# Kernel tuning notes

Hardware: AMD Instinct MI355X
Metric: run time of the kernel (lower is better)

The kernel has to match this reference:

```python
import jax, jax.numpy as jnp
import numpy as np

D_MODEL = 1024
NUM_HEADS = 4
KEY_DIM = 1024      # dim * expand_k
VALUE_DIM = 2048    # dim * expand_v
HEAD_QK = KEY_DIM // NUM_HEADS   # 256
HEAD_V = VALUE_DIM // NUM_HEADS  # 512
EPS = 1e-5
ROPE_BASE = 10000.0
XAVIER_GAIN = 2.0 ** (-2.5)


def _xavier_uniform(key, shape, gain=XAVIER_GAIN):
    fan_in, fan_out = shape
    a = gain * np.sqrt(6.0 / (fan_in + fan_out))
    return jax.random.uniform(key, shape, jnp.float32, -a, a)


def setup_inputs() -> dict:
    key = jax.random.key(0)
    ks = jax.random.split(key, 5)
    x = jax.random.normal(ks[0], (2, 2048, D_MODEL), jnp.float32)
    # stored as (in, out); y = x @ W matches torch Linear(no bias) with W^T
    Wq = _xavier_uniform(ks[1], (D_MODEL, KEY_DIM))
    Wk = _xavier_uniform(ks[2], (D_MODEL, KEY_DIM))
    Wv = _xavier_uniform(ks[3], (D_MODEL, VALUE_DIM))
    Wo = _xavier_uniform(ks[4], (VALUE_DIM, D_MODEL))
    return {"x": x, "Wq": Wq, "Wk": Wk, "Wv": Wv, "Wo": Wo}


def _rope(t, base=ROPE_BASE):
    # t: [b, n, h, d]; standard half-split rotary embedding
    n, d = t.shape[1], t.shape[-1]
    half = d // 2
    inv_freq = 1.0 / (base ** (jnp.arange(0, half, dtype=jnp.float32) * 2.0 / d))
    ang = jnp.arange(n, dtype=jnp.float32)[:, None] * inv_freq  # [n, d/2]
    cos = jnp.cos(ang)[None, :, None, :]
    sin = jnp.sin(ang)[None, :, None, :]
    t1, t2 = t[..., :half], t[..., half:]
    return jnp.concatenate([t1 * cos - t2 * sin, t2 * cos + t1 * sin], axis=-1)


def reference(x, Wq, Wk, Wv, Wo):
    b, n, _ = x.shape
    # projections: b n (h d) -> b (n) h d
    q = (x @ Wq).reshape(b, n, NUM_HEADS, HEAD_QK)
    k = (x @ Wk).reshape(b, n, NUM_HEADS, HEAD_QK)
    v = (x @ Wv).reshape(b, n, NUM_HEADS, HEAD_V).transpose(0, 2, 1, 3)  # b h n dv
    q = _rope(q).transpose(0, 2, 1, 3)  # b h n dk
    k = _rope(k).transpose(0, 2, 1, 3)
    scale = HEAD_QK ** (-0.5)
    exp_qk = jnp.tril(jnp.exp(jnp.einsum('bhid,bhjd->bhij', q, k) * scale))
    exp_kk = jnp.tril(jnp.exp(jnp.einsum('bhid,bhjd->bhij', k, k) * scale))
    A = exp_kk.astype(jnp.float32) + EPS * jnp.eye(n, dtype=jnp.float32)
    sol = jax.lax.linalg.triangular_solve(A, v.astype(jnp.float32),
                                          left_side=True, lower=True)
    o = exp_qk.astype(jnp.float32) @ sol                # b h n dv
    o = o.transpose(0, 2, 1, 3).reshape(b, n, VALUE_DIM)  # b n (h dv)
    return o.astype(x.dtype) @ Wo
```

## Files before the change

### kernel.cpp

```cpp
#include <hip/hip_runtime.h>
#include <hip/hip_bf16.h>
#include <math.h>

#define SEQ   2048
#define NROW  4096
#define DM    1024
#define LDQ   1024
#define LDV   2048
#define NBLK  16

typedef float  f32x4  __attribute__((ext_vector_type(4)));
typedef int    i32x4  __attribute__((ext_vector_type(4)));
typedef __bf16 bf16x8 __attribute__((ext_vector_type(8)));

#define MFMA(d, a, b) (d) = __builtin_amdgcn_mfma_f32_16x16x32_bf16((a), (b), (d), 0, 0, 0)

__device__ inline ushort f2bf(float f) {
  __hip_bfloat16 h = __float2bfloat16(f);
  return *(ushort*)&h;
}
__device__ inline float bf2f(ushort u) {
  return __uint_as_float((unsigned)u << 16);
}
__device__ inline void split2(float v, ushort& hi, ushort& lo) {
  hi = f2bf(v);
  lo = f2bf(v - bf2f(hi));
}
__device__ inline bf16x8 ldfrag(const ushort* p) { return *(const bf16x8*)p; }

__device__ inline void gload_lds16(const ushort* g, ushort* l) {
  __builtin_amdgcn_global_load_lds(
      (const __attribute__((address_space(1))) void*)g,
      (__attribute__((address_space(3))) void*)l, 16, 0, 0);
}

__global__ void pack_x_kernel(const float* __restrict__ X, ushort* __restrict__ P)
{
  const int t = blockIdx.x * 256 + threadIdx.x;
  const int kc = t & 127;
  const int m  = t >> 7;
  const float* src = X + (size_t)m * DM + kc * 8;
  f32x4 v0 = *(const f32x4*)src;
  f32x4 v1 = *(const f32x4*)(src + 4);
  ushort o[8];
  #pragma unroll
  for (int j = 0; j < 4; ++j) { o[j] = f2bf(v0[j]); o[4 + j] = f2bf(v1[j]); }
  ushort* dst = P + ((size_t)((m >> 7) * 128 + kc) * 128 + (m & 127)) * 8;
  *(i32x4*)dst = *(i32x4*)o;
}

__global__ void pack_w_kernel(const float* __restrict__ W, ushort* __restrict__ P,
                              int K, int N)
{
  const int K8 = K >> 3;
  const int t = blockIdx.x * 256 + threadIdx.x;
  const int c  = t & 127;
  const int kc = (t >> 7) % K8;
  const int nb = t / (128 * K8);
  ushort o[8];
  #pragma unroll
  for (int j = 0; j < 8; ++j)
    o[j] = f2bf(W[(size_t)(kc * 8 + j) * N + nb * 128 + c]);
  ushort* dst = P + ((size_t)(nb * K8 + kc) * 128 + c) * 8;
  *(i32x4*)dst = *(i32x4*)o;
}

__global__ void pack_w2_kernel(const float* __restrict__ Wq, const float* __restrict__ Wk,
                               ushort* __restrict__ Pq, ushort* __restrict__ Pk)
{
  const float* W = blockIdx.y ? Wk : Wq;
  ushort* P      = blockIdx.y ? Pk : Pq;
  const int K8 = 128;
  const int t = blockIdx.x * 256 + threadIdx.x;
  const int c  = t & 127;
  const int kc = (t >> 7) % K8;
  const int nb = t / (128 * K8);
  ushort o[8];
  #pragma unroll
  for (int j = 0; j < 8; ++j)
    o[j] = f2bf(W[(size_t)(kc * 8 + j) * 1024 + nb * 128 + c]);
  ushort* dst = P + ((size_t)(nb * K8 + kc) * 128 + c) * 8;
  *(i32x4*)dst = *(i32x4*)o;
}

__global__ void rope_pack1_kernel(const float* __restrict__ M,
                                  ushort* __restrict__ Phi, ushort* __restrict__ Plo)
{
  const int idx = blockIdx.x * 256 + threadIdx.x;
  const int g   = idx & 31;
  const int h   = (idx >> 5) & 3;
  const int row = idx >> 7;
  const int pos = row & (SEQ - 1);
  const int d0  = g * 8;
  const bool hihalf = d0 >= 128;
  const int f0 = d0 & 127;
  const float* mp = M + (size_t)row * LDQ + h * 256;
  ushort oh[8], ol[8];
  #pragma unroll
  for (int j = 0; j < 8; ++j) {
    const int f = f0 + j;
    const float inv = expf(-(float)f * (9.210340371976184f / 128.f));
    float s, c;
    sincosf((float)pos * inv, &s, &c);
    const float m1 = mp[f], m2 = mp[f + 128];
    const float mv = hihalf ? (m2 * c + m1 * s) : (m1 * c - m2 * s);
    split2(mv, oh[j], ol[j]);
  }
  const int b = row >> 11, r = row & 127, tb = (row & 2047) >> 7;
  const int bh = b * 4 + h;
  const size_t doff = (((size_t)(bh * 16 + tb) * 32 + g) * 128 + r) * 8;
  *(i32x4*)(Phi + doff) = *(i32x4*)oh;
  *(i32x4*)(Plo + doff) = *(i32x4*)ol;
}

__global__ void pack_sol_kernel(const float* __restrict__ Vb, ushort* __restrict__ Sp)
{
  const int hj = blockIdx.x;
  const int h  = hj >> 4, jb = hj & 15;
  const int c  = blockIdx.y * 256 + threadIdx.x;
  const float* src = Vb + (size_t)(jb * 128) * LDV + h * 512 + c;
  ushort* dhi = Sp + ((size_t)hj * 2    ) * 65536;
  ushort* dlo = Sp + ((size_t)hj * 2 + 1) * 65536;
  for (int kc = 0; kc < 16; ++kc) {
    ushort oh[8], ol[8];
    #pragma unroll
    for (int j = 0; j < 8; ++j)
      split2(src[(size_t)(kc * 8 + j) * LDV], oh[j], ol[j]);
    *(i32x4*)(dhi + ((size_t)kc * 512 + c) * 8) = *(i32x4*)oh;
    *(i32x4*)(dlo + ((size_t)kc * 512 + c) * 8) = *(i32x4*)ol;
  }
}

__global__ __launch_bounds__(256) void gemm_bf16(
    const ushort* __restrict__ Ap, const ushort* __restrict__ Bp,
    float* __restrict__ C, int M, int N, int K)
{
  __shared__ __align__(16) ushort a_lds[8][128][8];
  __shared__ __align__(16) ushort b_lds[8][128][8];
  const int tid  = threadIdx.x;
  const int lane = tid & 63;
  const int w    = tid >> 6;
  const int wr   = w >> 1, wc = w & 1;
  const int mb = blockIdx.y, nb = blockIdx.x;
  const int K8 = K >> 3;
  const ushort* aT = Ap + (size_t)mb * K8 * 1024;
  const ushort* bT = Bp + (size_t)nb * K8 * 1024;
  const int lr = lane & 15;
  const int lk = lane >> 4;

  f32x4 acc[4][4];
  #pragma unroll
  for (int i = 0; i < 4; ++i)
    #pragma unroll
    for (int j = 0; j < 4; ++j) acc[i][j] = (f32x4)(0.f);

  for (int kc0 = 0; kc0 < K8; kc0 += 8) {
    const ushort* asrc = aT + (size_t)kc0 * 1024;
    const ushort* bsrc = bT + (size_t)kc0 * 1024;
    __syncthreads();
    #pragma unroll
    for (int it = 0; it < 4; ++it) {
      gload_lds16(asrc + it * 2048 + tid * 8, ((ushort*)a_lds) + it * 2048 + tid * 8);
      gload_lds16(bsrc + it * 2048 + tid * 8, ((ushort*)b_lds) + it * 2048 + tid * 8);
    }
    __syncthreads();
    #pragma unroll
    for (int kk = 0; kk < 2; ++kk) {
      bf16x8 af[4], bf[4];
      #pragma unroll
      for (int m = 0; m < 4; ++m)
        af[m] = ldfrag(&a_lds[kk * 4 + lk][wr * 64 + m * 16 + lr][0]);
      #pragma unroll
      for (int n = 0; n < 4; ++n)
        bf[n] = ldfrag(&b_lds[kk * 4 + lk][wc * 64 + n * 16 + lr][0]);
      #pragma unroll
      for (int m = 0; m < 4; ++m)
        #pragma unroll
        for (int n = 0; n < 4; ++n)
          MFMA(acc[m][n], af[m], bf[n]);
    }
  }
  const int r0 = (lane >> 4) * 4;
  #pragma unroll
  for (int m = 0; m < 4; ++m)
    #pragma unroll
    for (int n = 0; n < 4; ++n) {
      const int row = mb * 128 + wr * 64 + m * 16 + r0;
      const int col = nb * 128 + wc * 64 + n * 16 + lr;
      float* cp = C + (size_t)row * N + col;
      #pragma unroll
      for (int q = 0; q < 4; ++q) cp[(size_t)q * N] = acc[m][n][q];
    }
}

__global__ __launch_bounds__(256) void winv_kernel(
    const ushort* __restrict__ Khi, const ushort* __restrict__ Klo,
    ushort* __restrict__ Whi, ushort* __restrict__ Wlo)
{
  __shared__ float L[128][129];
  __shared__ float W[128][129];
  const int t = blockIdx.x, bh = blockIdx.y;
  const int tid = threadIdx.x;
  const int lane = tid & 63, w = tid >> 6;
  const int wr = w >> 1, wc = w & 1;
  const int lr = lane & 15, lk = lane >> 4;
  const size_t kb = (size_t)(bh * 16 + t) * 32768;

  f32x4 acc[4][4];
  #pragma unroll
  for (int i = 0; i < 4; ++i)
    #pragma unroll
    for (int j = 0; j < 4; ++j) acc[i][j] = (f32x4)(0.f);
  #pragma unroll
  for (int ks = 0; ks < 8; ++ks) {
    bf16x8 ah[4], al[4];
    #pragma unroll
    for (int m = 0; m < 4; ++m) {
      const size_t off = kb + ((size_t)(ks * 4 + lk) * 128 + wr * 64 + m * 16 + lr) * 8;
      ah[m] = ldfrag(Khi + off);
      al[m] = ldfrag(Klo + off);
    }
    #pragma unroll
    for (int n = 0; n < 4; ++n) {
      const size_t off = kb + ((size_t)(ks * 4 + lk) * 128 + wc * 64 + n * 16 + lr) * 8;
      bf16x8 bh_ = ldfrag(Khi + off);
      bf16x8 bl_ = ldfrag(Klo + off);
      #pragma unroll
      for (int m = 0; m < 4; ++m) {
        MFMA(acc[m][n], ah[m], bh_);
        MFMA(acc[m][n], ah[m], bl_);
        MFMA(acc[m][n], al[m], bh_);
      }
    }
  }
  for (int i = tid; i < 128 * 129; i += 256) ((float*)W)[i] = 0.f;
  #pragma unroll
  for (int m = 0; m < 4; ++m)
    #pragma unroll
    for (int n = 0; n < 4; ++n)
      #pragma unroll
      for (int q = 0; q < 4; ++q) {
        const int row = wr * 64 + m * 16 + lk * 4 + q;
        const int col = wc * 64 + n * 16 + lr;
        float v = __expf(acc[m][n][q] * 0.0625f);
        if (row == col) v += 1e-5f;
        L[row][col] = v;
      }
  __syncthreads();
  if (tid < 128) {
    const int c = tid;
    W[c][c] = 1.f / L[c][c];
    for (int r = c + 1; r < 128; ++r) {
      float s0 = 0.f, s1 = 0.f, s2 = 0.f, s3 = 0.f;
      int j = c;
      for (; j + 4 <= r; j += 4) {
        s0 += L[r][j]     * W[j][c];
        s1 += L[r][j + 1] * W[j + 1][c];
        s2 += L[r][j + 2] * W[j + 2][c];
        s3 += L[r][j + 3] * W[j + 3][c];
      }
      for (; j < r; ++j) s0 += L[r][j] * W[j][c];
      W[r][c] = -((s0 + s1) + (s2 + s3)) / L[r][r];
    }
  }
  __syncthreads();
  const size_t wb = (size_t)(bh * 16 + t) * 16384;
  for (int i = tid; i < 2048; i += 256) {
    const int kc = i >> 7, r = i & 127;
    ushort oh[8], ol[8];
    #pragma unroll
    for (int j = 0; j < 8; ++j) split2(W[r][kc * 8 + j], oh[j], ol[j]);
    *(i32x4*)(Whi + wb + (size_t)i * 8) = *(i32x4*)oh;
    *(i32x4*)(Wlo + wb + (size_t)i * 8) = *(i32x4*)ol;
  }
}

__global__ __launch_bounds__(512) void apply_w0_kernel(
    const ushort* __restrict__ Whi, const ushort* __restrict__ Wlo,
    float* __restrict__ V, ushort* __restrict__ SR)
{
  __shared__ __align__(16) ushort shi[16 * 128 * 8];
  __shared__ __align__(16) ushort slo[16 * 128 * 8];
  const int cc = blockIdx.x, bh = blockIdx.y;
  const int b = bh >> 2, h = bh & 3;
  const int tid = threadIdx.x;
  const int lane = tid & 63, w = tid >> 6;
  const int wr = w >> 2, wc = w & 3, lr = lane & 15, lk = lane >> 4;
  const size_t wb = (size_t)(bh * 16) * 16384;
  float* Vrows = V + (size_t)b * SEQ * LDV + h * 512;
  ushort* srw = SR + (size_t)bh * 131072;

  {
    const int k = tid >> 2, c0 = (tid & 3) * 32;
    const float* vp = Vrows + (size_t)k * LDV + cc * 128 + c0;
    for (int c = 0; c < 32; ++c) {
      ushort hi, lo;
      split2(vp[c], hi, lo);
      const int idx = (((k >> 3) * 128) + c0 + c) * 8 + (k & 7);
      shi[idx] = hi; slo[idx] = lo;
    }
  }
  __syncthreads();
  f32x4 acc[4][2];
  #pragma unroll
  for (int i = 0; i < 4; ++i)
    #pragma unroll
    for (int j = 0; j < 2; ++j) acc[i][j] = (f32x4)(0.f);
  #pragma unroll
  for (int ks = 0; ks < 4; ++ks) {
    bf16x8 ah[4], al[4];
    #pragma unroll
    for (int m = 0; m < 4; ++m) {
      const size_t off = wb + ((size_t)(ks * 4 + lk) * 128 + wr * 64 + m * 16 + lr) * 8;
      ah[m] = ldfrag(Whi + off);
      al[m] = ldfrag(Wlo + off);
    }
    #pragma unroll
    for (int n = 0; n < 2; ++n) {
      const int idx = (((ks * 4 + lk) * 128) + wc * 32 + n * 16 + lr) * 8;
      bf16x8 bh_ = ldfrag(&shi[idx]);
      bf16x8 bl_ = ldfrag(&slo[idx]);
      #pragma unroll
      for (int m = 0; m < 4; ++m) {
        MFMA(acc[m][n], ah[m], bh_);
        MFMA(acc[m][n], ah[m], bl_);
        MFMA(acc[m][n], al[m], bh_);
      }
    }
  }
  #pragma unroll
  for (int m = 0; m < 4; ++m)
    #pragma unroll
    for (int n = 0; n < 2; ++n) {
      const int col = wc * 32 + n * 16 + lr;
      #pragma unroll
      for (int q = 0; q < 4; ++q) {
        const int row = wr * 64 + m * 16 + lk * 4 + q;
        const float v = acc[m][n][q];
        Vrows[(size_t)row * LDV + cc * 128 + col] = v;
        ushort hi, lo;
        split2(v, hi, lo);
        const size_t so = ((size_t)(row >> 3) * 512 + cc * 128 + col) * 8 + (row & 7);
        srw[so] = hi; srw[65536 + so] = lo;
      }
    }
}

__global__ __launch_bounds__(512) void solve_step_kernel(
    const ushort* __restrict__ Khi, const ushort* __restrict__ Klo,
    const ushort* __restrict__ Whi, const ushort* __restrict__ Wlo,
    float* __restrict__ V, ushort* __restrict__ SR, int t)
{
  __shared__ __align__(16) ushort pAhi[16 * 128 * 8];
  __shared__ __align__(16) ushort pAlo[16 * 128 * 8];
  const int ib = t + 1 + blockIdx.x;
  const int cc = blockIdx.y;
  const int bh = blockIdx.z;
  const int b = bh >> 2, h = bh & 3;
  const bool lead = (blockIdx.x == 0);
  const int tid = threadIdx.x;
  const int lane = tid & 63, w = tid >> 6;
  const int wr = w >> 2, wc = w & 3, lr = lane & 15, lk = lane >> 4;
  const size_t kbi = (size_t)(bh * 16 + ib) * 32768;
  const size_t kbt = (size_t)(bh * 16 + t) * 32768;
  float* Vhead = V + (size_t)b * SEQ * LDV + h * 512;
  float* Vib = Vhead + (size_t)ib * 128 * LDV;
  const ushort* srr = SR + (size_t)(t & 1) * 1048576 + (size_t)bh * 131072;
  ushort* srw       = SR + (size_t)((t + 1) & 1) * 1048576 + (size_t)bh * 131072;

  {
    f32x4 a1[4][2];
    #pragma unroll
    for (int i = 0; i < 4; ++i)
      #pragma unroll
      for (int j = 0; j < 2; ++j) a1[i][j] = (f32x4)(0.f);
    #pragma unroll
    for (int ks = 0; ks < 8; ++ks) {
      bf16x8 ah[4], al[4];
      #pragma unroll
      for (int m = 0; m < 4; ++m) {
        const size_t off = kbi + ((size_t)(ks * 4 + lk) * 128 + wr * 64 + m * 16 + lr) * 8;
        ah[m] = ldfrag(Khi + off);
        al[m] = ldfrag(Klo + off);
      }
      #pragma unroll
      for (int n = 0; n < 2; ++n) {
        const size_t off = kbt + ((size_t)(ks * 4 + lk) * 128 + wc * 32 + n * 16 + lr) * 8;
        bf16x8 bh_ = ldfrag(Khi + off);
        bf16x8 bl_ = ldfrag(Klo + off);
        #pragma unroll
        for (int m = 0; m < 4; ++m) {
          MFMA(a1[m][n], ah[m], bh_);
          MFMA(a1[m][n], ah[m], bl_);
          MFMA(a1[m][n], al[m], bh_);
        }
      }
    }
    #pragma unroll
    for (int m = 0; m < 4; ++m)
      #pragma unroll
      for (int n = 0; n < 2; ++n)
        #pragma unroll
        for (int q = 0; q < 4; ++q) {
          const int row = wr * 64 + m * 16 + lk * 4 + q;
          const int c   = wc * 32 + n * 16 + lr;
          const float e = __expf(a1[m][n][q] * 0.0625f);
          ushort hi, lo;
          split2(e, hi, lo);
          const int idx = (((c >> 3) * 128) + row) * 8 + (c & 7);
          pAhi[idx] = hi; pAlo[idx] = lo;
        }
  }
  __syncthreads();

  f32x4 u[4][2];
  #pragma unroll
  for (int i = 0; i < 4; ++i)
    #pragma unroll
    for (int j = 0; j < 2; ++j) u[i][j] = (f32x4)(0.f);
  #pragma unroll
  for (int ks = 0; ks < 4; ++ks) {
    bf16x8 ah[4], al[4];
    #pragma unroll
    for (int m = 0; m < 4; ++m) {
      const int idx = (((ks * 4 + lk) * 128) + wr * 64 + m * 16 + lr) * 8;
      ah[m] = ldfrag(&pAhi[idx]);
      al[m] = ldfrag(&pAlo[idx]);
    }
    #pragma unroll
    for (int n = 0; n < 2; ++n) {
      const size_t c = cc * 128 + wc * 32 + n * 16 + lr;
      bf16x8 bh_ = ldfrag(srr + ((size_t)(ks * 4 + lk) * 512 + c) * 8);
      bf16x8 bl_ = ldfrag(srr + 65536 + ((size_t)(ks * 4 + lk) * 512 + c) * 8);
      #pragma unroll
      for (int m = 0; m < 4; ++m) {
        MFMA(u[m][n], ah[m], bh_);
        MFMA(u[m][n], ah[m], bl_);
        MFMA(u[m][n], al[m], bh_);
      }
    }
  }
  float nv[4][2][4];
  #pragma unroll
  for (int m = 0; m < 4; ++m)
    #pragma unroll
    for (int n = 0; n < 2; ++n) {
      const int col = wc * 32 + n * 16 + lr;
      #pragma unroll
      for (int q = 0; q < 4; ++q) {
        const int row = wr * 64 + m * 16 + lk * 4 + q;
        const float v = Vib[(size_t)row * LDV + cc * 128 + col] - u[m][n][q];
        nv[m][n][q] = v;
        if (!lead) Vib[(size_t)row * LDV + cc * 128 + col] = v;
      }
    }
  if (lead) {
    __syncthreads();
    #pragma unroll
    for (int m = 0; m < 4; ++m)
      #pragma unroll
      for (int n = 0; n < 2; ++n) {
        const int col = wc * 32 + n * 16 + lr;
        #pragma unroll
        for (int q = 0; q < 4; ++q) {
          const int row = wr * 64 + m * 16 + lk * 4 + q;
          ushort hi, lo;
          split2(nv[m][n][q], hi, lo);
          const int idx = (((row >> 3) * 128) + col) * 8 + (row & 7);
          pAhi[idx] = hi; pAlo[idx] = lo;
        }
      }
    __syncthreads();
    f32x4 s2[4][2];
    #pragma unroll
    for (int i = 0; i < 4; ++i)
      #pragma unroll
      for (int j = 0; j < 2; ++j) s2[i][j] = (f32x4)(0.f);
    const size_t wb = (size_t)(bh * 16 + ib) * 16384;
    #pragma unroll
    for (int ks = 0; ks < 4; ++ks) {
      bf16x8 ah[4], al[4];
      #pragma unroll
      for (int m = 0; m < 4; ++m) {
        const size_t off = wb + ((size_t)(ks * 4 + lk) * 128 + wr * 64 + m * 16 + lr) * 8;
        ah[m] = ldfrag(Whi + off);
        al[m] = ldfrag(Wlo + off);
      }
      #pragma unroll
      for (int n = 0; n < 2; ++n) {
        const int idx = (((ks * 4 + lk) * 128) + wc * 32 + n * 16 + lr) * 8;
        bf16x8 bh_ = ldfrag(&pAhi[idx]);
        bf16x8 bl_ = ldfrag(&pAlo[idx]);
        #pragma unroll
        for (int m = 0; m < 4; ++m) {
          MFMA(s2[m][n], ah[m], bh_);
          MFMA(s2[m][n], ah[m], bl_);
          MFMA(s2[m][n], al[m], bh_);
        }
      }
    }
    #pragma unroll
    for (int m = 0; m < 4; ++m)
      #pragma unroll
      for (int n = 0; n < 2; ++n) {
        const int col = wc * 32 + n * 16 + lr;
        #pragma unroll
        for (int q = 0; q < 4; ++q) {
          const int row = wr * 64 + m * 16 + lk * 4 + q;
          const float v = s2[m][n][q];
          Vib[(size_t)row * LDV + cc * 128 + col] = v;
          ushort hi, lo;
          split2(v, hi, lo);
          const size_t so = ((size_t)(row >> 3) * 512 + cc * 128 + col) * 8 + (row & 7);
          srw[so] = hi; srw[65536 + so] = lo;
        }
      }
  }
}

__global__ __launch_bounds__(256, 4) void o_kernel(
    const ushort* __restrict__ Qhi, const ushort* __restrict__ Qlo,
    const ushort* __restrict__ Khi, const ushort* __restrict__ Klo,
    const ushort* __restrict__ Sp0, const ushort* __restrict__ Sp1,
    ushort* __restrict__ Opack)
{
  __shared__ __align__(16) ushort Phi_s[2][16 * 32 * 8];
  __shared__ __align__(16) ushort Plo_s[2][16 * 32 * 8];
  const int bid = blockIdx.x;
  const int bh  = bid & 7;
  const int rh  = (bid >> 3) & 3;
  const int ch  = (bid >> 5) & 1;
  const int ib  = 15 - (bid >> 6);
  const int b = bh >> 2, h = bh & 3;
  const int tid = threadIdx.x;
  const int lane = tid & 63;
  const int wv = tid >> 6;
  const int lr = lane & 15, lk = lane >> 4;
  const ushort* Spb = b ? Sp1 : Sp0;

  const size_t qb = (size_t)(bh * 16 + ib) * 32768;
  f32x4 acc[2][4];
  #pragma unroll
  for (int i = 0; i < 2; ++i)
    #pragma unroll
    for (int j = 0; j < 4; ++j) acc[i][j] = (f32x4)(0.f);

  int pb = 0;
  for (int jb = 0; jb <= ib; ++jb) {
    f32x4 s1[2][2];
    #pragma unroll
    for (int i = 0; i < 2; ++i)
      #pragma unroll
      for (int j = 0; j < 2; ++j) s1[i][j] = (f32x4)(0.f);
    const size_t kb = (size_t)(bh * 16 + jb) * 32768;
    __builtin_amdgcn_s_setprio(1);
    #pragma unroll
    for (int ks = 0; ks < 8; ++ks) {
      bf16x8 ah[2], al[2];
      #pragma unroll
      for (int m = 0; m < 2; ++m) {
        const size_t off = qb + ((size_t)(ks * 4 + lk) * 128 + rh * 32 + m * 16 + lr) * 8;
        ah[m] = ldfrag(Qhi + off);
        al[m] = ldfrag(Qlo + off);
      }
      #pragma unroll
      for (int n = 0; n < 2; ++n) {
        const size_t off = kb + ((size_t)(ks * 4 + lk) * 128 + wv * 32 + n * 16 + lr) * 8;
        bf16x8 bh_ = ldfrag(Khi + off);
        bf16x8 bl_ = ldfrag(Klo + off);
        #pragma unroll
        for (int m = 0; m < 2; ++m) {
          MFMA(s1[m][n], ah[m], bh_);
          MFMA(s1[m][n], ah[m], bl_);
          MFMA(s1[m][n], al[m], bh_);
        }
      }
    }
    __builtin_amdgcn_s_setprio(0);
    #pragma unroll
    for (int m = 0; m < 2; ++m)
      #pragma unroll
      for (int n = 0; n < 2; ++n)
        #pragma unroll
        for (int q = 0; q < 4; ++q) {
          const int rloc = m * 16 + lk * 4 + q;
          const int c    = wv * 32 + n * 16 + lr;
          float e = __expf(s1[m][n][q] * 0.0625f);
          if (jb == ib && c > rh * 32 + rloc) e = 0.f;
          ushort hi, lo;
          split2(e, hi, lo);
          const int idx = (((c >> 3) * 32) + rloc) * 8 + (c & 7);
          Phi_s[pb][idx] = hi; Plo_s[pb][idx] = lo;
        }
    __syncthreads();
    const ushort* sjb = Spb + ((size_t)(h * 16 + jb) * 2) * 65536;
    __builtin_amdgcn_s_setprio(1);
    #pragma unroll
    for (int ks = 0; ks < 4; ++ks) {
      bf16x8 ah[2], al[2];
      #pragma unroll
      for (int m = 0; m < 2; ++m) {
        const int idx = (((ks * 4 + lk) * 32) + m * 16 + lr) * 8;
        ah[m] = ldfrag(&Phi_s[pb][idx]);
        al[m] = ldfrag(&Plo_s[pb][idx]);
      }
      #pragma unroll
      for (int n = 0; n < 4; ++n) {
        const size_t c = ch * 256 + wv * 64 + n * 16 + lr;
        bf16x8 bh_ = ldfrag(sjb + ((size_t)(ks * 4 + lk) * 512 + c) * 8);
        bf16x8 bl_ = ldfrag(sjb + 65536 + ((size_t)(ks * 4 + lk) * 512 + c) * 8);
        #pragma unroll
        for (int m = 0; m < 2; ++m) {
          MFMA(acc[m][n], ah[m], bh_);
          MFMA(acc[m][n], ah[m], bl_);
          MFMA(acc[m][n], al[m], bh_);
        }
      }
    }
    __builtin_amdgcn_s_setprio(0);
    pb ^= 1;
  }
  const int row_blk = b * 16 + ib;
  #pragma unroll
  for (int m = 0; m < 2; ++m)
    #pragma unroll
    for (int n = 0; n < 4; ++n) {
      const int col = h * 512 + ch * 256 + wv * 64 + n * 16 + lr;
      #pragma unroll
      for (int q = 0; q < 4; ++q) {
        const int row = rh * 32 + m * 16 + lk * 4 + q;
        Opack[((size_t)row_blk * 256 + (col >> 3)) * 1024 + row * 8 + (col & 7)] =
            f2bf(acc[m][n][q]);
      }
    }
}

extern "C" void kernel_launch(void* const* d_in, const int* in_sizes, int n_in,
                              void* d_out, int out_size, void* d_ws, size_t ws_size,
                              hipStream_t stream)
{
  const float* x  = (const float*)d_in[0];
  const float* Wq = (const float*)d_in[1];
  const float* Wk = (const float*)d_in[2];
  const float* Wv = (const float*)d_in[3];
  const float* Wo = (const float*)d_in[4];
  float* out = (float*)d_out;

  char* base = (char*)d_ws;
  ushort* xpack = (ushort*)(base);
  ushort* Wqp   = (ushort*)(base + (8u  << 20));
  ushort* Wkp   = (ushort*)(base + (10u << 20));
  ushort* Wvp   = (ushort*)(base + (12u << 20));
  ushort* Wop   = (ushort*)(base + (16u << 20));
  float*  Q     = (float*) (base + (20u << 20));
  float*  K     = (float*) (base + (36u << 20));
  float*  V     = (float*) (base + (52u << 20));
  ushort* Qhi   = (ushort*)(base);
  ushort* Qlo   = (ushort*)(base + (8u  << 20));
  ushort* Khi   = (ushort*)(base + (20u << 20));
  ushort* Klo   = (ushort*)(base + (28u << 20));
  ushort* Whi   = (ushort*)(base + (36u << 20));
  ushort* Wlo   = (ushort*)(base + (40u << 20));
  ushort* SR    = (ushort*)(base + (44u << 20));
  ushort* Sp1   = (ushort*)(base + (36u << 20));
  ushort* Sp0   = (ushort*)(base + (68u << 20));
  ushort* Opack = (ushort*)(base + (52u << 20));

  pack_x_kernel<<<(NROW * 128) / 256, 256, 0, stream>>>(x, xpack);
  pack_w2_kernel<<<dim3((1024 * 1024 / 8) / 256, 2), 256, 0, stream>>>(Wq, Wk, Wqp, Wkp);
  pack_w_kernel<<<(1024 * 2048 / 8) / 256, 256, 0, stream>>>(Wv, Wvp, 1024, 2048);
  pack_w_kernel<<<(2048 * 1024 / 8) / 256, 256, 0, stream>>>(Wo, Wop, 2048, 1024);

  gemm_bf16<<<dim3(DM / 128, NROW / 128), 256, 0, stream>>>(xpack, Wqp, Q, NROW, DM, DM);
  gemm_bf16<<<dim3(DM / 128, NROW / 128), 256, 0, stream>>>(xpack, Wkp, K, NROW, DM, DM);
  gemm_bf16<<<dim3(LDV / 128, NROW / 128), 256, 0, stream>>>(xpack, Wvp, V, NROW, LDV, DM);

  rope_pack1_kernel<<<(NROW * 4 * 32) / 256, 256, 0, stream>>>(Q, Qhi, Qlo);
  rope_pack1_kernel<<<(NROW * 4 * 32) / 256, 256, 0, stream>>>(K, Khi, Klo);

  winv_kernel<<<dim3(NBLK, 8), 256, 0, stream>>>(Khi, Klo, Whi, Wlo);
  apply_w0_kernel<<<dim3(4, 8), 512, 0, stream>>>(Whi, Wlo, V, SR);
  for (int t = 0; t < NBLK - 1; ++t)
    solve_step_kernel<<<dim3(NBLK - 1 - t, 4, 8), 512, 0, stream>>>(Khi, Klo, Whi, Wlo, V, SR, t);

  pack_sol_kernel<<<dim3(64, 2), 256, 0, stream>>>(V + (size_t)SEQ * LDV, Sp1);
  pack_sol_kernel<<<dim3(64, 2), 256, 0, stream>>>(V, Sp0);

  o_kernel<<<1024, 256, 0, stream>>>(Qhi, Qlo, Khi, Klo, Sp0, Sp1, Opack);

  gemm_bf16<<<dim3(DM / 128, NROW / 128), 256, 0, stream>>>(Opack, Wop, out, NROW, DM, LDV);
}
```

Baseline: 1.269 ms.

## Process two diagonal blocks per launch in blocked triangular solve

The blocked forward substitution now advances two 128-row diagonal blocks per kernel launch instead of one. This cuts the serial chain from 15 step launches to 7, with block 1 folded into the initial apply kernel. Trailing blocks subtract both new solution panels in a single pass. The lead block does more serial work per launch: extra Gram recomputation, a chained solve for block B, and a 4-slot SR ring buffer that uses more scratch memory. The aim is to remove launch and grid-barrier overhead on the sequential critical path.

```diff
diff --git a/kernel.cpp b/kernel.cpp
--- a/kernel.cpp
+++ b/kernel.cpp
@@ -275,59 +275,203 @@
   }
 }
 
-__global__ __launch_bounds__(512) void apply_w0_kernel(
+__device__ inline void gram128(
+    const ushort* __restrict__ Khi, const ushort* __restrict__ Klo,
+    size_t kbi, size_t kbt, ushort* dhi, ushort* dlo,
+    int wr, int wc, int lr, int lk)
+{
+  f32x4 a1[4][2];
+  #pragma unroll
+  for (int i = 0; i < 4; ++i)
+    #pragma unroll
+    for (int j = 0; j < 2; ++j) a1[i][j] = (f32x4)(0.f);
+  #pragma unroll
+  for (int ks = 0; ks < 8; ++ks) {
+    bf16x8 ah[4], al[4];
+    #pragma unroll
+    for (int m = 0; m < 4; ++m) {
+      const size_t off = kbi + ((size_t)(ks * 4 + lk) * 128 + wr * 64 + m * 16 + lr) * 8;
+      ah[m] = ldfrag(Khi + off);
+      al[m] = ldfrag(Klo + off);
+    }
+    #pragma unroll
+    for (int n = 0; n < 2; ++n) {
+      const size_t off = kbt + ((size_t)(ks * 4 + lk) * 128 + wc * 32 + n * 16 + lr) * 8;
+      bf16x8 bh_ = ldfrag(Khi + off);
+      bf16x8 bl_ = ldfrag(Klo + off);
+      #pragma unroll
+      for (int m = 0; m < 4; ++m) {
+        MFMA(a1[m][n], ah[m], bh_);
+        MFMA(a1[m][n], ah[m], bl_);
+        MFMA(a1[m][n], al[m], bh_);
+      }
+    }
+  }
+  #pragma unroll
+  for (int m = 0; m < 4; ++m)
+    #pragma unroll
+    for (int n = 0; n < 2; ++n)
+      #pragma unroll
+      for (int q = 0; q < 4; ++q) {
+        const int row = wr * 64 + m * 16 + lk * 4 + q;
+        const int c   = wc * 32 + n * 16 + lr;
+        const float e = __expf(a1[m][n][q] * 0.0625f);
+        ushort hi, lo;
+        split2(e, hi, lo);
+        const int idx = (((c >> 3) * 128) + row) * 8 + (c & 7);
+        dhi[idx] = hi; dlo[idx] = lo;
+      }
+}
+
+__device__ inline void pv_acc(
+    const ushort* phi, const ushort* plo,
+    const ushort* bhi, const ushort* blo, int cstride, int cbase,
+    f32x4 (&u)[4][2], int wr, int wc, int lr, int lk)
+{
+  #pragma unroll
+  for (int ks = 0; ks < 4; ++ks) {
+    bf16x8 ah[4], al[4];
+    #pragma unroll
+    for (int m = 0; m < 4; ++m) {
+      const int idx = (((ks * 4 + lk) * 128) + wr * 64 + m * 16 + lr) * 8;
+      ah[m] = ldfrag(&phi[idx]);
+      al[m] = ldfrag(&plo[idx]);
+    }
+    #pragma unroll
+    for (int n = 0; n < 2; ++n) {
+      const size_t c = cbase + wc * 32 + n * 16 + lr;
+      bf16x8 bh_ = ldfrag(bhi + ((size_t)(ks * 4 + lk) * cstride + c) * 8);
+      bf16x8 bl_ = ldfrag(blo + ((size_t)(ks * 4 + lk) * cstride + c) * 8);
+      #pragma unroll
+      for (int m = 0; m < 4; ++m) {
+        MFMA(u[m][n], ah[m], bh_);
+        MFMA(u[m][n], ah[m], bl_);
+        MFMA(u[m][n], al[m], bh_);
+      }
+    }
+  }
+}
+
+__device__ inline void stage_bpack(
+    const f32x4 (&v)[4][2], ushort* dhi, ushort* dlo,
+    int wr, int wc, int lr, int lk)
+{
+  #pragma unroll
+  for (int m = 0; m < 4; ++m)
+    #pragma unroll
+    for (int n = 0; n < 2; ++n) {
+      const int col = wc * 32 + n * 16 + lr;
+      #pragma unroll
+      for (int q = 0; q < 4; ++q) {
+        const int row = wr * 64 + m * 16 + lk * 4 + q;
+        ushort hi, lo;
+        split2(v[m][n][q], hi, lo);
+        const int idx = (((row >> 3) * 128) + col) * 8 + (row & 7);
+        dhi[idx] = hi; dlo[idx] = lo;
+      }
+    }
+}
+
+__device__ inline void wapply(
+    const ushort* __restrict__ Whi, const ushort* __restrict__ Wlo, size_t wb,
+    const ushort* rhshi, const ushort* rhslo, f32x4 (&s2)[4][2],
+    int wr, int wc, int lr, int lk)
+{
+  #pragma unroll
+  for (int i = 0; i < 4; ++i)
+    #pragma unroll
+    for (int j = 0; j < 2; ++j) s2[i][j] = (f32x4)(0.f);
+  #pragma unroll
+  for (int ks = 0; ks < 4; ++ks) {
+    bf16x8 ah[4], al[4];
+    #pragma unroll
+    for (int m = 0; m < 4; ++m) {
+      const size_t off = wb + ((size_t)(ks * 4 + lk) * 128 + wr * 64 + m * 16 + lr) * 8;
+      ah[m] = ldfrag(Whi + off);
+      al[m] = ldfrag(Wlo + off);
+    }
+    #pragma unroll
+    for (int n = 0; n < 2; ++n) {
+      const int idx = (((ks * 4 + lk) * 128) + wc * 32 + n * 16 + lr) * 8;
+      bf16x8 bh_ = ldfrag(&rhshi[idx]);
+      bf16x8 bl_ = ldfrag(&rhslo[idx]);
+      #pragma unroll
+      for (int m = 0; m < 4; ++m) {
+        MFMA(s2[m][n], ah[m], bh_);
+        MFMA(s2[m][n], ah[m], bl_);
+        MFMA(s2[m][n], al[m], bh_);
+      }
+    }
+  }
+}
+
+__device__ inline void sol_out(
+    const f32x4 (&s2)[4][2], float* Vrow, ushort* srw, int cc,
+    int wr, int wc, int lr, int lk)
+{
+  #pragma unroll
+  for (int m = 0; m < 4; ++m)
+    #pragma unroll
+    for (int n = 0; n < 2; ++n) {
+      const int col = wc * 32 + n * 16 + lr;
+      #pragma unroll
+      for (int q = 0; q < 4; ++q) {
+        const int row = wr * 64 + m * 16 + lk * 4 + q;
+        const float v = s2[m][n][q];
+        Vrow[(size_t)row * LDV + cc * 128 + col] = v;
+        ushort hi, lo;
+        split2(v, hi, lo);
+        const size_t so = ((size_t)(row >> 3) * 512 + cc * 128 + col) * 8 + (row & 7);
+        srw[so] = hi; srw[65536 + so] = lo;
+      }
+    }
+}
+
+#define SR_SLOT(s) (SR + (size_t)((s) & 3) * 1048576 + (size_t)bh * 131072)
+
+__global__ __launch_bounds__(512) void apply_w01_kernel(
+    const ushort* __restrict__ Khi, const ushort* __restrict__ Klo,
     const ushort* __restrict__ Whi, const ushort* __restrict__ Wlo,
     float* __restrict__ V, ushort* __restrict__ SR)
 {
-  __shared__ __align__(16) ushort shi[16 * 128 * 8];
-  __shared__ __align__(16) ushort slo[16 * 128 * 8];
+  __shared__ __align__(16) ushort pAhi[16 * 128 * 8];
+  __shared__ __align__(16) ushort pAlo[16 * 128 * 8];
+  __shared__ __align__(16) ushort pBhi[16 * 128 * 8];
+  __shared__ __align__(16) ushort pBlo[16 * 128 * 8];
   const int cc = blockIdx.x, bh = blockIdx.y;
   const int b = bh >> 2, h = bh & 3;
   const int tid = threadIdx.x;
   const int lane = tid & 63, w = tid >> 6;
   const int wr = w >> 2, wc = w & 3, lr = lane & 15, lk = lane >> 4;
-  const size_t wb = (size_t)(bh * 16) * 16384;
-  float* Vrows = V + (size_t)b * SEQ * LDV + h * 512;
-  ushort* srw = SR + (size_t)bh * 131072;
+  float* Vhead = V + (size_t)b * SEQ * LDV + h * 512;
+  float* V1 = Vhead + (size_t)128 * LDV;
 
   {
     const int k = tid >> 2, c0 = (tid & 3) * 32;
-    const float* vp = Vrows + (size_t)k * LDV + cc * 128 + c0;
+    const float* vp = Vhead + (size_t)k * LDV + cc * 128 + c0;
     for (int c = 0; c < 32; ++c) {
       ushort hi, lo;
       split2(vp[c], hi, lo);
       const int idx = (((k >> 3) * 128) + c0 + c) * 8 + (k & 7);
-      shi[idx] = hi; slo[idx] = lo;
-    }
-  }
-  __syncthreads();
-  f32x4 acc[4][2];
+      pAhi[idx] = hi; pAlo[idx] = lo;
+    }
+  }
+  __syncthreads();
+  f32x4 s2[4][2];
+  wapply(Whi, Wlo, (size_t)(bh * 16) * 16384, pAhi, pAlo, s2, wr, wc, lr, lk);
+  sol_out(s2, Vhead, SR_SLOT(0), cc, wr, wc, lr, lk);
+  __syncthreads();
+  stage_bpack(s2, pBhi, pBlo, wr, wc, lr, lk);
+  gram128(Khi, Klo, (size_t)(bh * 16 + 1) * 32768, (size_t)(bh * 16) * 32768,
+          pAhi, pAlo, wr, wc, lr, lk);
+  __syncthreads();
+  f32x4 u[4][2];
   #pragma unroll
   for (int i = 0; i < 4; ++i)
     #pragma unroll
-    for (int j = 0; j < 2; ++j) acc[i][j] = (f32x4)(0.f);
-  #pragma unroll
-  for (int ks = 0; ks < 4; ++ks) {
-    bf16x8 ah[4], al[4];
-    #pragma unroll
-    for (int m = 0; m < 4; ++m) {
-      const size_t off = wb + ((size_t)(ks * 4 + lk) * 128 + wr * 64 + m * 16 + lr) * 8;
-      ah[m] = ldfrag(Whi + off);
-      al[m] = ldfrag(Wlo + off);
-    }
-    #pragma unroll
-    for (int n = 0; n < 2; ++n) {
-      const int idx = (((ks * 4 + lk) * 128) + wc * 32 + n * 16 + lr) * 8;
-      bf16x8 bh_ = ldfrag(&shi[idx]);
-      bf16x8 bl_ = ldfrag(&slo[idx]);
-      #pragma unroll
-      for (int m = 0; m < 4; ++m) {
-        MFMA(acc[m][n], ah[m], bh_);
-        MFMA(acc[m][n], ah[m], bl_);
-        MFMA(acc[m][n], al[m], bh_);
-      }
-    }
-  }
+    for (int j = 0; j < 2; ++j) u[i][j] = (f32x4)(0.f);
+  pv_acc(pAhi, pAlo, pBhi, pBlo, 128, 0, u, wr, wc, lr, lk);
+  f32x4 nv[4][2];
   #pragma unroll
   for (int m = 0; m < 4; ++m)
     #pragma unroll
@@ -336,126 +480,50 @@
       #pragma unroll
       for (int q = 0; q < 4; ++q) {
         const int row = wr * 64 + m * 16 + lk * 4 + q;
-        const float v = acc[m][n][q];
-        Vrows[(size_t)row * LDV + cc * 128 + col] = v;
-        ushort hi, lo;
-        split2(v, hi, lo);
-        const size_t so = ((size_t)(row >> 3) * 512 + cc * 128 + col) * 8 + (row & 7);
-        srw[so] = hi; srw[65536 + so] = lo;
-      }
-    }
-}
-
-__global__ __launch_bounds__(512) void solve_step_kernel(
+        nv[m][n][q] = V1[(size_t)row * LDV + cc * 128 + col] - u[m][n][q];
+      }
+    }
+  __syncthreads();
+  stage_bpack(nv, pAhi, pAlo, wr, wc, lr, lk);
+  __syncthreads();
+  wapply(Whi, Wlo, (size_t)(bh * 16 + 1) * 16384, pAhi, pAlo, s2, wr, wc, lr, lk);
+  sol_out(s2, V1, SR_SLOT(1), cc, wr, wc, lr, lk);
+}
+
+__global__ __launch_bounds__(512) void solve_step2_kernel(
     const ushort* __restrict__ Khi, const ushort* __restrict__ Klo,
     const ushort* __restrict__ Whi, const ushort* __restrict__ Wlo,
-    float* __restrict__ V, ushort* __restrict__ SR, int t)
+    float* __restrict__ V, ushort* __restrict__ SR, int p)
 {
   __shared__ __align__(16) ushort pAhi[16 * 128 * 8];
   __shared__ __align__(16) ushort pAlo[16 * 128 * 8];
-  const int ib = t + 1 + blockIdx.x;
-  const int cc = blockIdx.y;
-  const int bh = blockIdx.z;
+  __shared__ __align__(16) ushort pBhi[16 * 128 * 8];
+  __shared__ __align__(16) ushort pBlo[16 * 128 * 8];
+  const int bx = blockIdx.x, cc = blockIdx.y, bh = blockIdx.z;
   const int b = bh >> 2, h = bh & 3;
-  const bool lead = (blockIdx.x == 0);
   const int tid = threadIdx.x;
   const int lane = tid & 63, w = tid >> 6;
   const int wr = w >> 2, wc = w & 3, lr = lane & 15, lk = lane >> 4;
-  const size_t kbi = (size_t)(bh * 16 + ib) * 32768;
-  const size_t kbt = (size_t)(bh * 16 + t) * 32768;
+  const int s0 = 2 * p, s1 = 2 * p + 1, A = 2 * p + 2, B = 2 * p + 3;
   float* Vhead = V + (size_t)b * SEQ * LDV + h * 512;
-  float* Vib = Vhead + (size_t)ib * 128 * LDV;
-  const ushort* srr = SR + (size_t)(t & 1) * 1048576 + (size_t)bh * 131072;
-  ushort* srw       = SR + (size_t)((t + 1) & 1) * 1048576 + (size_t)bh * 131072;
-
-  {
-    f32x4 a1[4][2];
+  const ushort* sr0 = SR_SLOT(s0);
+  const ushort* sr1 = SR_SLOT(s1);
+  #define KB(x) ((size_t)(bh * 16 + (x)) * 32768)
+  #define WB(x) ((size_t)(bh * 16 + (x)) * 16384)
+
+  if (bx >= 1) {
+    const int ib = B + bx;
+    float* Vib = Vhead + (size_t)(ib * 128) * LDV;
+    gram128(Khi, Klo, KB(ib), KB(s0), pAhi, pAlo, wr, wc, lr, lk);
+    gram128(Khi, Klo, KB(ib), KB(s1), pBhi, pBlo, wr, wc, lr, lk);
+    __syncthreads();
+    f32x4 u[4][2];
     #pragma unroll
     for (int i = 0; i < 4; ++i)
       #pragma unroll
-      for (int j = 0; j < 2; ++j) a1[i][j] = (f32x4)(0.f);
-    #pragma unroll
-    for (int ks = 0; ks < 8; ++ks) {
-      bf16x8 ah[4], al[4];
-      #pragma unroll
-      for (int m = 0; m < 4; ++m) {
-        const size_t off = kbi + ((size_t)(ks * 4 + lk) * 128 + wr * 64 + m * 16 + lr) * 8;
-        ah[m] = ldfrag(Khi + off);
-        al[m] = ldfrag(Klo + off);
-      }
-      #pragma unroll
-      for (int n = 0; n < 2; ++n) {
-        const size_t off = kbt + ((size_t)(ks * 4 + lk) * 128 + wc * 32 + n * 16 + lr) * 8;
-        bf16x8 bh_ = ldfrag(Khi + off);
-        bf16x8 bl_ = ldfrag(Klo + off);
-        #pragma unroll
-        for (int m = 0; m < 4; ++m) {
-          MFMA(a1[m][n], ah[m], bh_);
-          MFMA(a1[m][n], ah[m], bl_);
-          MFMA(a1[m][n], al[m], bh_);
-        }
-      }
-    }
-    #pragma unroll
-    for (int m = 0; m < 4; ++m)
-      #pragma unroll
-      for (int n = 0; n < 2; ++n)
-        #pragma unroll
-        for (int q = 0; q < 4; ++q) {
-          const int row = wr * 64 + m * 16 + lk * 4 + q;
-          const int c   = wc * 32 + n * 16 + lr;
-          const float e = __expf(a1[m][n][q] * 0.0625f);
-          ushort hi, lo;
-          split2(e, hi, lo);
-          const int idx = (((c >> 3) * 128) + row) * 8 + (c & 7);
-          pAhi[idx] = hi; pAlo[idx] = lo;
-        }
-  }
-  __syncthreads();
-
-  f32x4 u[4][2];
-  #pragma unroll
-  for (int i = 0; i < 4; ++i)
-    #pragma unroll
-    for (int j = 0; j < 2; ++j) u[i][j] = (f32x4)(0.f);
-  #pragma unroll
-  for (int ks = 0; ks < 4; ++ks) {
-    bf16x8 ah[4], al[4];
-    #pragma unroll
-    for (int m = 0; m < 4; ++m) {
-      const int idx = (((ks * 4 + lk) * 128) + wr * 64 + m * 16 + lr) * 8;
-      ah[m] = ldfrag(&pAhi[idx]);
-      al[m] = ldfrag(&pAlo[idx]);
-    }
-    #pragma unroll
-    for (int n = 0; n < 2; ++n) {
-      const size_t c = cc * 128 + wc * 32 + n * 16 + lr;
-      bf16x8 bh_ = ldfrag(srr + ((size_t)(ks * 4 + lk) * 512 + c) * 8);
-      bf16x8 bl_ = ldfrag(srr + 65536 + ((size_t)(ks * 4 + lk) * 512 + c) * 8);
-      #pragma unroll
-      for (int m = 0; m < 4; ++m) {
-        MFMA(u[m][n], ah[m], bh_);
-        MFMA(u[m][n], ah[m], bl_);
-        MFMA(u[m][n], al[m], bh_);
-      }
-    }
-  }
-  float nv[4][2][4];
-  #pragma unroll
-  for (int m = 0; m < 4; ++m)
-    #pragma unroll
-    for (int n = 0; n < 2; ++n) {
-      const int col = wc * 32 + n * 16 + lr;
-      #pragma unroll
-      for (int q = 0; q < 4; ++q) {
-        const int row = wr * 64 + m * 16 + lk * 4 + q;
-        const float v = Vib[(size_t)row * LDV + cc * 128 + col] - u[m][n][q];
-        nv[m][n][q] = v;
-        if (!lead) Vib[(size_t)row * LDV + cc * 128 + col] = v;
-      }
-    }
-  if (lead) {
-    __syncthreads();
+      for (int j = 0; j < 2; ++j) u[i][j] = (f32x4)(0.f);
+    pv_acc(pAhi, pAlo, sr0, sr0 + 65536, 512, cc * 128, u, wr, wc, lr, lk);
+    pv_acc(pBhi, pBlo, sr1, sr1 + 65536, 512, cc * 128, u, wr, wc, lr, lk);
     #pragma unroll
     for (int m = 0; m < 4; ++m)
       #pragma unroll
@@ -464,58 +532,78 @@
         #pragma unroll
         for (int q = 0; q < 4; ++q) {
           const int row = wr * 64 + m * 16 + lk * 4 + q;
-          ushort hi, lo;
-          split2(nv[m][n][q], hi, lo);
-          const int idx = (((row >> 3) * 128) + col) * 8 + (row & 7);
-          pAhi[idx] = hi; pAlo[idx] = lo;
+          float* ptr = &Vib[(size_t)row * LDV + cc * 128 + col];
+          *ptr = *ptr - u[m][n][q];
         }
       }
-    __syncthreads();
-    f32x4 s2[4][2];
-    #pragma unroll
-    for (int i = 0; i < 4; ++i)
-      #pragma unroll
-      for (int j = 0; j < 2; ++j) s2[i][j] = (f32x4)(0.f);
-    const size_t wb = (size_t)(bh * 16 + ib) * 16384;
-    #pragma unroll
-    for (int ks = 0; ks < 4; ++ks) {
-      bf16x8 ah[4], al[4];
-      #pragma unroll
-      for (int m = 0; m < 4; ++m) {
-        const size_t off = wb + ((size_t)(ks * 4 + lk) * 128 + wr * 64 + m * 16 + lr) * 8;
-        ah[m] = ldfrag(Whi + off);
-        al[m] = ldfrag(Wlo + off);
-      }
-      #pragma unroll
-      for (int n = 0; n < 2; ++n) {
-        const int idx = (((ks * 4 + lk) * 128) + wc * 32 + n * 16 + lr) * 8;
-        bf16x8 bh_ = ldfrag(&pAhi[idx]);
-        bf16x8 bl_ = ldfrag(&pAlo[idx]);
-        #pragma unroll
-        for (int m = 0; m < 4; ++m) {
-          MFMA(s2[m][n], ah[m], bh_);
-          MFMA(s2[m][n], ah[m], bl_);
-          MFMA(s2[m][n], al[m], bh_);
-        }
-      }
-    }
-    #pragma unroll
-    for (int m = 0; m < 4; ++m)
-      #pragma unroll
-      for (int n = 0; n < 2; ++n) {
-        const int col = wc * 32 + n * 16 + lr;
-        #pragma unroll
-        for (int q = 0; q < 4; ++q) {
-          const int row = wr * 64 + m * 16 + lk * 4 + q;
-          const float v = s2[m][n][q];
-          Vib[(size_t)row * LDV + cc * 128 + col] = v;
-          ushort hi, lo;
-          split2(v, hi, lo);
-          const size_t so = ((size_t)(row >> 3) * 512 + cc * 128 + col) * 8 + (row & 7);
-          srw[so] = hi; srw[65536 + so] = lo;
-        }
-      }
-  }
+    return;
+  }
+
+  float* VA = Vhead + (size_t)(A * 128) * LDV;
+  float* VB = Vhead + (size_t)(B * 128) * LDV;
+  f32x4 u[4][2], nv[4][2], s2[4][2];
+
+  gram128(Khi, Klo, KB(A), KB(s0), pAhi, pAlo, wr, wc, lr, lk);
+  gram128(Khi, Klo, KB(A), KB(s1), pBhi, pBlo, wr, wc, lr, lk);
+  __syncthreads();
+  #pragma unroll
+  for (int i = 0; i < 4; ++i)
+    #pragma unroll
+    for (int j = 0; j < 2; ++j) u[i][j] = (f32x4)(0.f);
+  pv_acc(pAhi, pAlo, sr0, sr0 + 65536, 512, cc * 128, u, wr, wc, lr, lk);
+  pv_acc(pBhi, pBlo, sr1, sr1 + 65536, 512, cc * 128, u, wr, wc, lr, lk);
+  #pragma unroll
+  for (int m = 0; m < 4; ++m)
+    #pragma unroll
+    for (int n = 0; n < 2; ++n) {
+      const int col = wc * 32 + n * 16 + lr;
+      #pragma unroll
+      for (int q = 0; q < 4; ++q) {
+        const int row = wr * 64 + m * 16 + lk * 4 + q;
+        nv[m][n][q] = VA[(size_t)row * LDV + cc * 128 + col] - u[m][n][q];
+      }
+    }
+  __syncthreads();
+  stage_bpack(nv, pAhi, pAlo, wr, wc, lr, lk);
+  __syncthreads();
+  wapply(Whi, Wlo, WB(A), pAhi, pAlo, s2, wr, wc, lr, lk);
+  sol_out(s2, VA, SR_SLOT(A), cc, wr, wc, lr, lk);
+  __syncthreads();
+  stage_bpack(s2, pBhi, pBlo, wr, wc, lr, lk);
+
+  gram128(Khi, Klo, KB(B), KB(s0), pAhi, pAlo, wr, wc, lr, lk);
+  __syncthreads();
+  #pragma unroll
+  for (int i = 0; i < 4; ++i)
+    #pragma unroll
+    for (int j = 0; j < 2; ++j) u[i][j] = (f32x4)(0.f);
+  pv_acc(pAhi, pAlo, sr0, sr0 + 65536, 512, cc * 128, u, wr, wc, lr, lk);
+  __syncthreads();
+  gram128(Khi, Klo, KB(B), KB(s1), pAhi, pAlo, wr, wc, lr, lk);
+  __syncthreads();
+  pv_acc(pAhi, pAlo, sr1, sr1 + 65536, 512, cc * 128, u, wr, wc, lr, lk);
+  __syncthreads();
+  gram128(Khi, Klo, KB(B), KB(A), pAhi, pAlo, wr, wc, lr, lk);
+  __syncthreads();
+  pv_acc(pAhi, pAlo, pBhi, pBlo, 128, 0, u, wr, wc, lr, lk);
+  #pragma unroll
+  for (int m = 0; m < 4; ++m)
+    #pragma unroll
+    for (int n = 0; n < 2; ++n) {
+      const int col = wc * 32 + n * 16 + lr;
+      #pragma unroll
+      for (int q = 0; q < 4; ++q) {
+        const int row = wr * 64 + m * 16 + lk * 4 + q;
+        nv[m][n][q] = VB[(size_t)row * LDV + cc * 128 + col] - u[m][n][q];
+      }
+    }
+  __syncthreads();
+  stage_bpack(nv, pAhi, pAlo, wr, wc, lr, lk);
+  __syncthreads();
+  wapply(Whi, Wlo, WB(B), pAhi, pAlo, s2, wr, wc, lr, lk);
+  sol_out(s2, VB, SR_SLOT(B), cc, wr, wc, lr, lk);
+  #undef KB
+  #undef WB
 }
 
 __global__ __launch_bounds__(256, 4) void o_kernel(
@@ -679,9 +767,10 @@
   rope_pack1_kernel<<<(NROW * 4 * 32) / 256, 256, 0, stream>>>(K, Khi, Klo);
 
   winv_kernel<<<dim3(NBLK, 8), 256, 0, stream>>>(Khi, Klo, Whi, Wlo);
-  apply_w0_kernel<<<dim3(4, 8), 512, 0, stream>>>(Whi, Wlo, V, SR);
-  for (int t = 0; t < NBLK - 1; ++t)
-    solve_step_kernel<<<dim3(NBLK - 1 - t, 4, 8), 512, 0, stream>>>(Khi, Klo, Whi, Wlo, V, SR, t);
+  apply_w01_kernel<<<dim3(4, 8), 512, 0, stream>>>(Khi, Klo, Whi, Wlo, V, SR);
+  for (int p = 0; p < 7; ++p)
+    solve_step2_kernel<<<dim3(13 - 2 * p, 4, 8), 512, 0, stream>>>(
+        Khi, Klo, Whi, Wlo, V, SR, p);
 
   pack_sol_kernel<<<dim3(64, 2), 256, 0, stream>>>(V + (size_t)SEQ * LDV, Sp1);
   pack_sol_kernel<<<dim3(64, 2), 256, 0, stream>>>(V, Sp0);
```

Result: slower. 1.817 ms (+43.2%).
